# Kernel optimization log

Hardware: AMD Instinct MI355X
Metric: run time of the kernel (lower is better)

Reference implementation:

```python
import jax, jax.numpy as jnp
import numpy as np

CUBIC_A = -0.75  # torch bicubic coefficient


def _cubic_weights(t):
    # torch get_cubic_upsample_coefficients, t in [0,1): weights for taps at -1,0,1,2
    A = CUBIC_A
    def c1(x):
        return ((A + 2.0) * x - (A + 3.0)) * x * x + 1.0
    def c2(x):
        return ((A * x - 5.0 * A) * x + 8.0 * A) * x - 4.0 * A
    return jnp.stack([c2(t + 1.0), c1(t), c1(1.0 - t), c2(2.0 - t)])  # [4, ...]


def geo_cyclic_pad(x, p):
    # GeoCyclicPadding: pole rows are flipped and shifted by half the longitudes,
    # longitude is padded cyclically.
    B, C, H, W = x.shape
    top = jnp.roll(jnp.flip(x[:, :, :p, :], axis=2), W // 2, axis=3)
    bot = jnp.roll(jnp.flip(x[:, :, H - p:, :], axis=2), W // 2, axis=3)
    x = jnp.concatenate([top, x, bot], axis=2)
    x = jnp.concatenate([x[:, :, :, -p:], x, x[:, :, :, :p]], axis=3)
    return x


def bicubic_grid_sample(img, gx, gy):
    # img: [N, Hp, Wp]; gx, gy: [N, Ho, Wo] normalized coords in [-1, 1]
    # torch grid_sample(mode='bicubic', align_corners=True, padding_mode='border')
    N, Hp, Wp = img.shape
    ix = (gx + 1.0) * 0.5 * (Wp - 1)
    iy = (gy + 1.0) * 0.5 * (Hp - 1)
    ix0 = jnp.floor(ix)
    iy0 = jnp.floor(iy)
    tx = ix - ix0
    ty = iy - iy0
    wx = _cubic_weights(tx)  # [4, N, Ho, Wo]
    wy = _cubic_weights(ty)  # [4, N, Ho, Wo]
    offs = jnp.arange(-1, 3, dtype=jnp.int32)[:, None, None, None]
    xs = jnp.clip(ix0.astype(jnp.int32)[None] + offs, 0, Wp - 1)  # [4,N,Ho,Wo] (border)
    ys = jnp.clip(iy0.astype(jnp.int32)[None] + offs, 0, Hp - 1)
    n = jnp.arange(N, dtype=jnp.int32)[None, None, :, None, None]
    vals = img[n, ys[:, None], xs[None, :]]  # [4, 4, N, Ho, Wo]
    return jnp.einsum('jnhw,inhw,jinhw->nhw', wy, wx, vals)


def reference(hidden_features, lat_grid, lon_grid, W_vel, b_vel, dt):
    B, C, H, W = hidden_features.shape
    two_pi = 2.0 * jnp.pi
    # velocity net (pointwise conv hidden_dim -> 2*hidden_dim)
    vel = jnp.einsum('bchw,oc->bohw', hidden_features, W_vel) + b_vel[None, :, None, None]
    vel = vel.reshape(B, 2, C, H, W)
    u, v = vel[:, 0], vel[:, 1]
    lon_prime = -u * dt
    lat_prime = -v * dt
    lat_p = lat_grid[:, None]  # [B,1,H,W] broadcasts over C
    lon_p = lon_grid[:, None]
    # rotated -> standard lat/lon
    slp, clp = jnp.sin(lat_prime), jnp.cos(lat_prime)
    slo, clo = jnp.sin(lon_prime), jnp.cos(lon_prime)
    sp, cp = jnp.sin(lat_p), jnp.cos(lat_p)
    sin_lat = slp * cp + clp * clo * sp
    lat = jnp.arcsin(jnp.clip(sin_lat, -1.0 + 1e-7, 1.0 - 1e-7))
    num = clp * slo
    den = clp * clo * cp - slp * sp
    lon = jnp.remainder(lon_p + jnp.arctan2(num, den) + two_pi, two_pi)
    min_lat, max_lat = jnp.min(lat_grid), jnp.max(lat_grid)
    min_lon, max_lon = jnp.min(lon_grid), jnp.max(lon_grid)
    gx = 2.0 * (lon - min_lon) / (max_lon - min_lon) - 1.0
    gy = 2.0 * (lat - min_lat) / (max_lat - min_lat) - 1.0
    # periodic wrap in longitude, pole reflection in latitude
    gx = jnp.remainder(gx + 1.0, 2.0) - 1.0
    left = gx <= 0.0
    outer = jnp.abs(gy) > 1.0
    gx = jnp.where(outer & left, gx + 1.0, gx)
    gx = jnp.where(outer & (~left), gx - 1.0, gx)
    gy = jnp.where(gy < -1.0, -(2.0 + gy), gy)
    gy = jnp.where(gy > 1.0, 2.0 - gy, gy)
    # pad and rescale grid to padded size (align_corners=True)
    padded = geo_cyclic_pad(hidden_features, 1)  # [B,C,H+2,W+2]
    Hp, Wp = H + 2, W + 2
    gx = gx * (W / Wp)
    gy = gy * (H / Hp)
    img = padded.reshape(B * C, Hp, Wp)
    out = bicubic_grid_sample(img, gx.reshape(B * C, H, W), gy.reshape(B * C, H, W))
    return out.reshape(B, C, H, W)


def setup_inputs() -> dict:
    key = jax.random.key(0)
    k1, k2 = jax.random.split(key, 2)
    B, C, H, W = 2, 64, 180, 360
    hidden_features = jax.random.normal(k1, (B, C, H, W), dtype=jnp.float32)
    lat = jnp.linspace(-jnp.pi / 2, jnp.pi / 2, H, dtype=jnp.float32)
    lon = jnp.arange(W, dtype=jnp.float32) * (2.0 * jnp.pi / W)
    lat_grid = jnp.broadcast_to(lat[:, None], (H, W))
    lon_grid = jnp.broadcast_to(lon[None, :], (H, W))
    lat_grid = jnp.broadcast_to(lat_grid[None], (B, H, W)).astype(jnp.float32)
    lon_grid = jnp.broadcast_to(lon_grid[None], (B, H, W)).astype(jnp.float32)
    W_vel = jax.random.normal(k2, (2 * C, C), dtype=jnp.float32) * 0.02
    b_vel = jnp.zeros((2 * C,), dtype=jnp.float32)
    return {"hidden_features": hidden_features, "lat_grid": lat_grid,
            "lon_grid": lon_grid, "W_vel": W_vel, "b_vel": b_vel, "dt": 1.0}
```

## Files before the change

### kernel.cpp

```cpp
#include <hip/hip_runtime.h>
#include <math.h>

constexpr int B_ = 2, C_ = 64, H_ = 180, W_ = 360;
constexpr int HW = H_ * W_;
constexpr int Hp = H_ + 2, Wp = W_ + 2;
constexpr int O_ = 2 * C_;

__device__ __forceinline__ float frem(float x, float y) {
    return x - floorf(x / y) * y;
}
__device__ __forceinline__ float frem2(float x) {
    return x - floorf(x * 0.5f) * 2.0f;
}

__device__ __forceinline__ float cub1(float x) {
    return (1.25f * x - 2.25f) * x * x + 1.0f;
}
__device__ __forceinline__ float cub2(float x) {
    return ((-0.75f * x + 3.75f) * x - 6.0f) * x + 3.0f;
}

__device__ __forceinline__ float fetch_pad(const float* __restrict__ img, int y, int x) {
    int wc = x - 1;
    if (x == 0)      wc = W_ - 1;
    if (x == Wp - 1) wc = 0;
    int hh = y - 1;
    bool top = (y == 0), bot = (y == Hp - 1);
    if (top) hh = 0;
    if (bot) hh = H_ - 1;
    if (top || bot) { wc += W_ / 2; if (wc >= W_) wc -= W_; }
    return img[hh * W_ + wc];
}

__device__ __forceinline__ float advect_one(
    const float* __restrict__ img,
    float u, float v, float dt,
    float sp, float cp, float lon_p,
    float min_lat, float min_lon, float inv_dlat, float inv_dlon)
{
    const float two_pi = 6.28318530717958647f;
    const float sxw = (float)W_ / (float)Wp;
    const float syh = (float)H_ / (float)Hp;

    const float lon_pr = -u * dt;
    const float lat_pr = -v * dt;
    float slp, clp, slo, clo;
    __sincosf(lat_pr, &slp, &clp);
    __sincosf(lon_pr, &slo, &clo);
    float sin_lat = slp * cp + clp * clo * sp;
    sin_lat = fminf(fmaxf(sin_lat, -1.0f + 1e-7f), 1.0f - 1e-7f);
    const float lat = asinf(sin_lat);
    const float num = clp * slo;
    const float den = clp * clo * cp - slp * sp;
    const float lon = frem(lon_p + atan2f(num, den) + two_pi, two_pi);

    float gx = (lon - min_lon) * inv_dlon - 1.0f;
    float gy = (lat - min_lat) * inv_dlat - 1.0f;
    gx = frem2(gx + 1.0f) - 1.0f;
    const bool left  = (gx <= 0.0f);
    const bool outer = (fabsf(gy) > 1.0f);
    if (outer) gx += left ? 1.0f : -1.0f;
    if (gy < -1.0f)     gy = -(2.0f + gy);
    else if (gy > 1.0f) gy = 2.0f - gy;
    gx *= sxw;
    gy *= syh;

    const float ix = (gx + 1.0f) * 0.5f * (float)(Wp - 1);
    const float iy = (gy + 1.0f) * 0.5f * (float)(Hp - 1);
    const float fx0 = floorf(ix), fy0 = floorf(iy);
    const float tx = ix - fx0, ty = iy - fy0;
    const int jx = (int)fx0, jy = (int)fy0;

    float t[16];
    const bool interior = (jx >= 2) & (jx <= Wp - 4) & (jy >= 2) & (jy <= Hp - 4);
    if (__all(interior)) {
        const float* __restrict__ p = img + (jy - 2) * W_ + (jx - 2);
#pragma unroll
        for (int r = 0; r < 4; ++r)
#pragma unroll
            for (int cc = 0; cc < 4; ++cc)
                t[r * 4 + cc] = p[r * W_ + cc];
    } else {
        int xs[4], ys[4];
#pragma unroll
        for (int r = 0; r < 4; ++r) {
            xs[r] = min(max(jx - 1 + r, 0), Wp - 1);
            ys[r] = min(max(jy - 1 + r, 0), Hp - 1);
        }
#pragma unroll
        for (int r = 0; r < 4; ++r)
#pragma unroll
            for (int cc = 0; cc < 4; ++cc)
                t[r * 4 + cc] = fetch_pad(img, ys[r], xs[cc]);
    }

    const float wx0 = cub2(tx + 1.0f), wx1 = cub1(tx);
    const float wx2 = cub1(1.0f - tx), wx3 = cub2(2.0f - tx);
    const float wy0 = cub2(ty + 1.0f), wy1 = cub1(ty);
    const float wy2 = cub1(1.0f - ty), wy3 = cub2(2.0f - ty);

    const float r0 = fmaf(wx3, t[3],  fmaf(wx2, t[2],  fmaf(wx1, t[1],  wx0 * t[0])));
    const float r1 = fmaf(wx3, t[7],  fmaf(wx2, t[6],  fmaf(wx1, t[5],  wx0 * t[4])));
    const float r2 = fmaf(wx3, t[11], fmaf(wx2, t[10], fmaf(wx1, t[9],  wx0 * t[8])));
    const float r3 = fmaf(wx3, t[15], fmaf(wx2, t[14], fmaf(wx1, t[13], wx0 * t[12])));

    return fmaf(wy3, r3, fmaf(wy2, r2, fmaf(wy1, r1, wy0 * r0)));
}

constexpr int P1_PXT = 256;
constexpr int P1_OG  = 2;
constexpr int P1_OPG = O_ / P1_OG;
constexpr int P1_TILES = (HW + P1_PXT - 1) / P1_PXT;

__global__ __launch_bounds__(P1_PXT, 4) void nsl_vel(
    const float* __restrict__ hidden, const float* __restrict__ W_vel,
    const float* __restrict__ b_vel, float* __restrict__ uv)
{
    const int bid  = blockIdx.x;
    const int tile = bid % P1_TILES;
    const int og   = (bid / P1_TILES) % P1_OG;
    const int b    = bid / (P1_TILES * P1_OG);
    const int px   = tile * P1_PXT + threadIdx.x;
    if (px >= HW) return;

    float acc[P1_OPG];
#pragma unroll
    for (int j = 0; j < P1_OPG; ++j) acc[j] = b_vel[og * P1_OPG + j];

    const float* hb = hidden + (size_t)b * C_ * HW + px;
    const float* Wg = W_vel + (size_t)og * P1_OPG * C_;

    float xf[4];
#pragma unroll
    for (int t = 0; t < 4; ++t) xf[t] = hb[(size_t)t * HW];

    for (int k0 = 0; k0 < C_; k0 += 4) {
        float xc[4];
#pragma unroll
        for (int t = 0; t < 4; ++t) xc[t] = xf[t];
        if (k0 + 4 < C_) {
#pragma unroll
            for (int t = 0; t < 4; ++t) xf[t] = hb[(size_t)(k0 + 4 + t) * HW];
        }
#pragma unroll
        for (int j = 0; j < P1_OPG; ++j) {
            const float* wr = Wg + (size_t)j * C_ + k0;
            acc[j] = fmaf(wr[0], xc[0], acc[j]);
            acc[j] = fmaf(wr[1], xc[1], acc[j]);
            acc[j] = fmaf(wr[2], xc[2], acc[j]);
            acc[j] = fmaf(wr[3], xc[3], acc[j]);
        }
    }

    float* o = uv + ((size_t)b * O_ + og * P1_OPG) * HW + px;
#pragma unroll
    for (int j = 0; j < P1_OPG; ++j) o[(size_t)j * HW] = acc[j];
}

__global__ __launch_bounds__(256, 6) void nsl_advect(
    const float* __restrict__ hidden,
    const float* __restrict__ lat_grid,
    const float* __restrict__ lon_grid,
    const float* __restrict__ uv,
    const float* __restrict__ dt_p,
    float* __restrict__ out)
{
    const int idx = blockIdx.x * 256 + threadIdx.x;
    if (idx >= B_ * C_ * HW) return;
    const int px = idx % HW;
    const int bc = idx / HW;
    const int b  = bc / C_;
    const int c  = bc - b * C_;

    const float dt      = dt_p[0];
    const float min_lat = lat_grid[0];
    const float max_lat = lat_grid[(H_ - 1) * W_];
    const float min_lon = lon_grid[0];
    const float max_lon = lon_grid[W_ - 1];
    const float inv_dlat = 2.0f / (max_lat - min_lat);
    const float inv_dlon = 2.0f / (max_lon - min_lon);

    const float lat_p = lat_grid[(size_t)b * HW + px];
    const float lon_p = lon_grid[(size_t)b * HW + px];
    float sp, cp;
    __sincosf(lat_p, &sp, &cp);

    const float u = uv[((size_t)b * O_ + c) * HW + px];
    const float v = uv[((size_t)b * O_ + C_ + c) * HW + px];

    const float* __restrict__ img = hidden + (size_t)bc * HW;
    out[(size_t)bc * HW + px] = advect_one(img, u, v, dt, sp, cp, lon_p,
                                           min_lat, min_lon, inv_dlat, inv_dlon);
}

constexpr int FB_CG = 4, FB_CPT = C_ / FB_CG, FB_PXT = 256;
constexpr int FB_TILES = (HW + FB_PXT - 1) / FB_PXT;

__global__ __launch_bounds__(FB_PXT, 6) void nsl_fused(
    const float* __restrict__ hidden, const float* __restrict__ lat_grid,
    const float* __restrict__ lon_grid, const float* __restrict__ W_vel,
    const float* __restrict__ b_vel, const float* __restrict__ dt_p,
    float* __restrict__ out)
{
    const int bid  = blockIdx.x;
    const int tile = bid % FB_TILES;
    const int cg   = (bid / FB_TILES) % FB_CG;
    const int b    = bid / (FB_TILES * FB_CG);
    const int px   = tile * FB_PXT + threadIdx.x;
    if (px >= HW) return;

    const float dt      = dt_p[0];
    const float min_lat = lat_grid[0];
    const float max_lat = lat_grid[(H_ - 1) * W_];
    const float min_lon = lon_grid[0];
    const float max_lon = lon_grid[W_ - 1];
    const float inv_dlat = 2.0f / (max_lat - min_lat);
    const float inv_dlon = 2.0f / (max_lon - min_lon);

    const float lat_p = lat_grid[(size_t)b * HW + px];
    const float lon_p = lon_grid[(size_t)b * HW + px];
    float sp, cp;
    __sincosf(lat_p, &sp, &cp);

    float u[FB_CPT], v[FB_CPT];
#pragma unroll
    for (int i = 0; i < FB_CPT; ++i) {
        u[i] = b_vel[cg * FB_CPT + i];
        v[i] = b_vel[C_ + cg * FB_CPT + i];
    }
    const float* hb = hidden + (size_t)b * C_ * HW + px;
#pragma unroll 2
    for (int k = 0; k < C_; ++k) {
        const float x = hb[(size_t)k * HW];
#pragma unroll
        for (int i = 0; i < FB_CPT; ++i) {
            u[i] = fmaf(W_vel[(size_t)(cg * FB_CPT + i) * C_ + k], x, u[i]);
            v[i] = fmaf(W_vel[(size_t)(C_ + cg * FB_CPT + i) * C_ + k], x, v[i]);
        }
    }

    for (int i = 0; i < FB_CPT; ++i) {
        const int c = cg * FB_CPT + i;
        const float* __restrict__ img = hidden + ((size_t)b * C_ + c) * HW;
        out[((size_t)b * C_ + c) * HW + px] =
            advect_one(img, u[i], v[i], dt, sp, cp, lon_p,
                       min_lat, min_lon, inv_dlat, inv_dlon);
    }
}

extern "C" void kernel_launch(void* const* d_in, const int* in_sizes, int n_in,
                              void* d_out, int out_size, void* d_ws, size_t ws_size,
                              hipStream_t stream) {
    const float* hidden   = (const float*)d_in[0];
    const float* lat_grid = (const float*)d_in[1];
    const float* lon_grid = (const float*)d_in[2];
    const float* W_vel    = (const float*)d_in[3];
    const float* b_vel    = (const float*)d_in[4];
    const float* dt_p     = (const float*)d_in[5];
    float* out = (float*)d_out;

    const size_t uv_bytes = (size_t)B_ * O_ * HW * sizeof(float);
    if (ws_size >= uv_bytes) {
        float* uv = (float*)d_ws;
        nsl_vel<<<B_ * P1_OG * P1_TILES, P1_PXT, 0, stream>>>(hidden, W_vel, b_vel, uv);
        const int n2 = B_ * C_ * HW;
        nsl_advect<<<(n2 + 255) / 256, 256, 0, stream>>>(hidden, lat_grid, lon_grid,
                                                         uv, dt_p, out);
    } else {
        nsl_fused<<<B_ * FB_CG * FB_TILES, FB_PXT, 0, stream>>>(
            hidden, lat_grid, lon_grid, W_vel, b_vel, dt_p, out);
    }
}
```

Baseline: 239.4 us.

## Register-tile the velocity pointwise conv as an 8x8 outer product per thread

Rewrites the velocity projection kernel so each thread computes 8 output channels for 8 consecutive pixels. It uses float4 loads of the hidden features and the weights, and float4 stores of the uv result. This replaces the one-pixel-per-thread, 64-outputs-per-thread scheme that read hidden twice across two output groups. The aim is more reuse per load and fewer, wider memory instructions. The cost is higher register pressure (a 64-float accumulator, with launch bounds lowered to 3), and hidden tiles are reread from cache by the 16 channel-group threads.

```diff
diff --git a/kernel.cpp b/kernel.cpp
--- a/kernel.cpp
+++ b/kernel.cpp
@@ -107,54 +107,62 @@
     return fmaf(wy3, r3, fmaf(wy2, r2, fmaf(wy1, r1, wy0 * r0)));
 }
 
-constexpr int P1_PXT = 256;
-constexpr int P1_OG  = 2;
-constexpr int P1_OPG = O_ / P1_OG;
-constexpr int P1_TILES = (HW + P1_PXT - 1) / P1_PXT;
-
-__global__ __launch_bounds__(P1_PXT, 4) void nsl_vel(
+constexpr int V_JPT  = 8;
+constexpr int V_PPT  = 8;
+constexpr int V_TILE = 16 * V_PPT;
+constexpr int V_TILES = (HW + V_TILE - 1) / V_TILE;
+
+__global__ __launch_bounds__(256, 3) void nsl_vel(
     const float* __restrict__ hidden, const float* __restrict__ W_vel,
     const float* __restrict__ b_vel, float* __restrict__ uv)
 {
     const int bid  = blockIdx.x;
-    const int tile = bid % P1_TILES;
-    const int og   = (bid / P1_TILES) % P1_OG;
-    const int b    = bid / (P1_TILES * P1_OG);
-    const int px   = tile * P1_PXT + threadIdx.x;
+    const int tile = bid % V_TILES;
+    const int b    = bid / V_TILES;
+    const int tid  = threadIdx.x;
+    const int jt   = tid >> 4;
+    const int pt   = tid & 15;
+    const int j0   = jt * V_JPT;
+    const int px   = tile * V_TILE + pt * V_PPT;
     if (px >= HW) return;
 
-    float acc[P1_OPG];
-#pragma unroll
-    for (int j = 0; j < P1_OPG; ++j) acc[j] = b_vel[og * P1_OPG + j];
+    float acc[V_JPT][V_PPT];
+#pragma unroll
+    for (int jj = 0; jj < V_JPT; ++jj) {
+        const float bj = b_vel[j0 + jj];
+#pragma unroll
+        for (int p = 0; p < V_PPT; ++p) acc[jj][p] = bj;
+    }
 
     const float* hb = hidden + (size_t)b * C_ * HW + px;
-    const float* Wg = W_vel + (size_t)og * P1_OPG * C_;
-
-    float xf[4];
-#pragma unroll
-    for (int t = 0; t < 4; ++t) xf[t] = hb[(size_t)t * HW];
-
-    for (int k0 = 0; k0 < C_; k0 += 4) {
-        float xc[4];
-#pragma unroll
-        for (int t = 0; t < 4; ++t) xc[t] = xf[t];
-        if (k0 + 4 < C_) {
-#pragma unroll
-            for (int t = 0; t < 4; ++t) xf[t] = hb[(size_t)(k0 + 4 + t) * HW];
+
+#pragma unroll 1
+    for (int k = 0; k < C_; k += 4) {
+        float xv[4][8];
+#pragma unroll
+        for (int kk = 0; kk < 4; ++kk) {
+            *(float4*)&xv[kk][0] = *(const float4*)(hb + (size_t)(k + kk) * HW);
+            *(float4*)&xv[kk][4] = *(const float4*)(hb + (size_t)(k + kk) * HW + 4);
         }
-#pragma unroll
-        for (int j = 0; j < P1_OPG; ++j) {
-            const float* wr = Wg + (size_t)j * C_ + k0;
-            acc[j] = fmaf(wr[0], xc[0], acc[j]);
-            acc[j] = fmaf(wr[1], xc[1], acc[j]);
-            acc[j] = fmaf(wr[2], xc[2], acc[j]);
-            acc[j] = fmaf(wr[3], xc[3], acc[j]);
-        }
-    }
-
-    float* o = uv + ((size_t)b * O_ + og * P1_OPG) * HW + px;
-#pragma unroll
-    for (int j = 0; j < P1_OPG; ++j) o[(size_t)j * HW] = acc[j];
+        float wv[V_JPT][4];
+#pragma unroll
+        for (int jj = 0; jj < V_JPT; ++jj)
+            *(float4*)&wv[jj][0] = *(const float4*)(W_vel + (size_t)(j0 + jj) * C_ + k);
+#pragma unroll
+        for (int jj = 0; jj < V_JPT; ++jj)
+#pragma unroll
+            for (int kk = 0; kk < 4; ++kk)
+#pragma unroll
+                for (int p = 0; p < V_PPT; ++p)
+                    acc[jj][p] = fmaf(wv[jj][kk], xv[kk][p], acc[jj][p]);
+    }
+
+    float* o = uv + ((size_t)b * O_ + j0) * HW + px;
+#pragma unroll
+    for (int jj = 0; jj < V_JPT; ++jj) {
+        *(float4*)(o + (size_t)jj * HW)     = *(float4*)&acc[jj][0];
+        *(float4*)(o + (size_t)jj * HW + 4) = *(float4*)&acc[jj][4];
+    }
 }
 
 __global__ __launch_bounds__(256, 6) void nsl_advect(
@@ -262,7 +270,7 @@
     const size_t uv_bytes = (size_t)B_ * O_ * HW * sizeof(float);
     if (ws_size >= uv_bytes) {
         float* uv = (float*)d_ws;
-        nsl_vel<<<B_ * P1_OG * P1_TILES, P1_PXT, 0, stream>>>(hidden, W_vel, b_vel, uv);
+        nsl_vel<<<B_ * V_TILES, 256, 0, stream>>>(hidden, W_vel, b_vel, uv);
         const int n2 = B_ * C_ * HW;
         nsl_advect<<<(n2 + 255) / 256, 256, 0, stream>>>(hidden, lat_grid, lon_grid,
                                                          uv, dt_p, out);
```

After: 243.7 us. About the same (+1.8%).
